# Kernel optimization log

Measured on AMD Instinct MI355X. Metric: run time of the kernel, lower is better.

## Reference

```python
import jax, jax.numpy as jnp
import numpy as np

H = 4  # hidden_size
L = 2  # num_layers


def _lstm_cell(x, h, c, Wih, Whh, bih, bhh):
    # PyTorch gate order: input, forget, cell(g), output
    gates = x @ Wih.T + h @ Whh.T + (bih + bhh)  # [B, 4H]
    i, f, g, o = jnp.split(gates, 4, axis=-1)
    i = jax.nn.sigmoid(i)
    f = jax.nn.sigmoid(f)
    g = jnp.tanh(g)
    o = jax.nn.sigmoid(o)
    c_new = f * c + i * g
    h_new = o * jnp.tanh(c_new)
    return h_new, c_new


def setup_inputs() -> dict:
    key = jax.random.key(0)
    ks = jax.random.split(key, 24)
    B, S, D, T = 32768, 256, 8, 12
    s = 1.0 / np.sqrt(H)  # PyTorch LSTM init scale

    def u(k, shape):
        return jax.random.uniform(k, shape, jnp.float32, -s, s)

    inp = {
        "src": jax.random.normal(ks[0], (B, S, D), jnp.float32),
        "trg": jax.random.normal(ks[1], (B, T, 1), jnp.float32),
        # encoder LSTM (input_dim=8 -> H, then H -> H)
        "enc_Wih0": u(ks[2], (4 * H, D)), "enc_Whh0": u(ks[3], (4 * H, H)),
        "enc_bih0": u(ks[4], (4 * H,)), "enc_bhh0": u(ks[5], (4 * H,)),
        "enc_Wih1": u(ks[6], (4 * H, H)), "enc_Whh1": u(ks[7], (4 * H, H)),
        "enc_bih1": u(ks[8], (4 * H,)), "enc_bhh1": u(ks[9], (4 * H,)),
        # decoder LSTM (input_dim=1 -> H, then H -> H)
        "dec_Wih0": u(ks[10], (4 * H, 1)), "dec_Whh0": u(ks[11], (4 * H, H)),
        "dec_bih0": u(ks[12], (4 * H,)), "dec_bhh0": u(ks[13], (4 * H,)),
        "dec_Wih1": u(ks[14], (4 * H, H)), "dec_Whh1": u(ks[15], (4 * H, H)),
        "dec_bih1": u(ks[16], (4 * H,)), "dec_bhh1": u(ks[17], (4 * H,)),
        # fc: hidden -> 1
        "fc_W": u(ks[18], (1, H)), "fc_b": u(ks[19], (1,)),
    }
    return inp


def reference(src, trg,
              enc_Wih0, enc_Whh0, enc_bih0, enc_bhh0,
              enc_Wih1, enc_Whh1, enc_bih1, enc_bhh1,
              dec_Wih0, dec_Whh0, dec_bih0, dec_bhh0,
              dec_Wih1, dec_Whh1, dec_bih1, dec_bhh1,
              fc_W, fc_b):
    B, T = src.shape[0], trg.shape[1]
    enc_layers = [(enc_Wih0, enc_Whh0, enc_bih0, enc_bhh0),
                  (enc_Wih1, enc_Whh1, enc_bih1, enc_bhh1)]
    dec_layers = [(dec_Wih0, dec_Whh0, dec_bih0, dec_bhh0),
                  (dec_Wih1, dec_Whh1, dec_bih1, dec_bhh1)]

    def multi_step(layers, h, c, x):
        new_h, new_c, inp = [], [], x
        for l, p in enumerate(layers):
            hl, cl = _lstm_cell(inp, h[l], c[l], *p)
            new_h.append(hl); new_c.append(cl); inp = hl
        return jnp.stack(new_h), jnp.stack(new_c), inp

    # ---- encoder: scan over src time steps ----
    h0 = jnp.zeros((L, B, H), src.dtype)
    c0 = jnp.zeros((L, B, H), src.dtype)

    def enc_step(carry, x_t):
        h, c = carry
        h, c, _ = multi_step(enc_layers, h, c, x_t)
        return (h, c), None

    (h, c), _ = jax.lax.scan(enc_step, (h0, c0), jnp.swapaxes(src, 0, 1))

    x0 = trg[:, 0, :]  # [B, 1]

    def dec_step(carry, _):
        h, c, x = carry
        h, c, top = multi_step(dec_layers, h, c, x)
        pred = top @ fc_W.T + fc_b  # [B, 1]
        return (h, c, pred), pred

    _, preds = jax.lax.scan(dec_step, (h, c, x0), None, length=T - 1)  # [T-1, B, 1]
    outputs = jnp.concatenate([x0[None], preds], axis=0)  # [T, B, 1]
    return jnp.swapaxes(outputs, 0, 1)  # [B, T, 1]
```

## Files before the change

### kernel.cpp

```cpp
#include <hip/hip_runtime.h>

namespace {

constexpr int Sn = 256;
constexpr int Tn = 12;
constexpr float L2E = 1.44269504088896340736f;

typedef float v2f __attribute__((ext_vector_type(2)));

__device__ __forceinline__ v2f pkfma(v2f a, v2f b, v2f c) {
  return __builtin_elementwise_fma(a, b, c);
}

__device__ __forceinline__ float rcp_(float x) { return __builtin_amdgcn_rcpf(x); }

#if __has_builtin(__builtin_amdgcn_exp2f)
__device__ __forceinline__ float exp2_(float x) { return __builtin_amdgcn_exp2f(x); }
#else
__device__ __forceinline__ float exp2_(float x) { return __expf(x * 0.69314718055994530942f); }
#endif

template <int CTRL>
__device__ __forceinline__ float qperm(float v) {
  return __int_as_float(
      __builtin_amdgcn_mov_dpp(__float_as_int(v), CTRL, 0xF, 0xF, true));
}
constexpr int DPP_XOR1 = 0xB1;
constexpr int DPP_XOR2 = 0x4E;
constexpr int DPP_XOR3 = 0x1B;
constexpr int DPP_BC0 = 0x00;

__device__ __forceinline__ float unit_update(v2f g01, v2f g23, float& c) {
  float iv = rcp_(1.0f + exp2_(g01.x));
  float fv = rcp_(1.0f + exp2_(g01.y));
  float gv = fmaf(-2.0f, rcp_(exp2_(g23.x) + 1.0f), 1.0f);
  float ov = rcp_(1.0f + exp2_(g23.y));
  c = fmaf(fv, c, iv * gv);
  float th = fmaf(-2.0f, rcp_(exp2_(c * (2.0f * L2E)) + 1.0f), 1.0f);
  return ov * th;
}

__device__ __forceinline__ void quad_gather(float h, float* hg) {
  hg[0] = h;
  hg[1] = qperm<DPP_XOR1>(h);
  hg[2] = qperm<DPP_XOR2>(h);
  hg[3] = qperm<DPP_XOR3>(h);
}

__global__ __launch_bounds__(64, 2) void seq2seq_kernel(
    const float* __restrict__ src, const float* __restrict__ trg,
    const float* __restrict__ eWih0, const float* __restrict__ eWhh0,
    const float* __restrict__ ebih0, const float* __restrict__ ebhh0,
    const float* __restrict__ eWih1, const float* __restrict__ eWhh1,
    const float* __restrict__ ebih1, const float* __restrict__ ebhh1,
    const float* __restrict__ dWih0, const float* __restrict__ dWhh0,
    const float* __restrict__ dbih0, const float* __restrict__ dbhh0,
    const float* __restrict__ dWih1, const float* __restrict__ dWhh1,
    const float* __restrict__ dbih1, const float* __restrict__ dbhh1,
    const float* __restrict__ fcW, const float* __restrict__ fcb,
    float* __restrict__ out) {
  const int gid = blockIdx.x * 64 + threadIdx.x;
  const int e = gid >> 2;
  const int u = gid & 3;

  const int ri = u, rf = 4 + u, rg = 8 + u, ro = 12 + u;

  const v2f s01 = v2f{-L2E, -L2E};
  const v2f s23 = v2f{2.0f * L2E, -L2E};

  v2f w0x01[8], w0x23[8], w0h01[4], w0h23[4];
  v2f w1i01[4], w1i23[4], w1h01[4], w1h23[4];
#pragma unroll
  for (int j = 0; j < 8; ++j) {
    w0x01[j] = v2f{eWih0[ri * 8 + j], eWih0[rf * 8 + j]} * s01;
    w0x23[j] = v2f{eWih0[rg * 8 + j], eWih0[ro * 8 + j]} * s23;
  }
#pragma unroll
  for (int k = 0; k < 4; ++k) {
    const int kc = u ^ k;
    w0h01[k] = v2f{eWhh0[ri * 4 + kc], eWhh0[rf * 4 + kc]} * s01;
    w0h23[k] = v2f{eWhh0[rg * 4 + kc], eWhh0[ro * 4 + kc]} * s23;
    w1i01[k] = v2f{eWih1[ri * 4 + kc], eWih1[rf * 4 + kc]} * s01;
    w1i23[k] = v2f{eWih1[rg * 4 + kc], eWih1[ro * 4 + kc]} * s23;
    w1h01[k] = v2f{eWhh1[ri * 4 + kc], eWhh1[rf * 4 + kc]} * s01;
    w1h23[k] = v2f{eWhh1[rg * 4 + kc], eWhh1[ro * 4 + kc]} * s23;
  }
  const v2f b0_01 = v2f{ebih0[ri] + ebhh0[ri], ebih0[rf] + ebhh0[rf]} * s01;
  const v2f b0_23 = v2f{ebih0[rg] + ebhh0[rg], ebih0[ro] + ebhh0[ro]} * s23;
  const v2f b1_01 = v2f{ebih1[ri] + ebhh1[ri], ebih1[rf] + ebhh1[rf]} * s01;
  const v2f b1_23 = v2f{ebih1[rg] + ebhh1[rg], ebih1[ro] + ebhh1[ro]} * s23;

  const float4* sp = (const float4*)(src + (size_t)e * (Sn * 8));

  float h0g[4] = {0, 0, 0, 0};
  float h1g[4] = {0, 0, 0, 0};
  float c0 = 0.0f, c1 = 0.0f;

  v2f xA01[8], xA23[8], xB01[8], xB23[8];
  float4 raw[16];

  auto convert = [&](int r, v2f& o01, v2f& o23) {
    float4 xa = raw[2 * r], xb = raw[2 * r + 1];
    float x[8] = {xa.x, xa.y, xa.z, xa.w, xb.x, xb.y, xb.z, xb.w};
    v2f a01 = b0_01, a23 = b0_23;
#pragma unroll
    for (int j = 0; j < 8; ++j) {
      v2f xx = v2f{x[j], x[j]};
      a01 = pkfma(xx, w0x01[j], a01);
      a23 = pkfma(xx, w0x23[j], a23);
    }
    o01 = a01;
    o23 = a23;
  };

  auto rstep = [&](v2f a01, v2f a23) {
#pragma unroll
    for (int k = 0; k < 4; ++k) {
      v2f hh = v2f{h0g[k], h0g[k]};
      a01 = pkfma(hh, w0h01[k], a01);
      a23 = pkfma(hh, w0h23[k], a23);
    }
    float h0 = unit_update(a01, a23, c0);
    quad_gather(h0, h0g);

    v2f e01 = b1_01, e23 = b1_23;
#pragma unroll
    for (int k = 0; k < 4; ++k) {
      v2f hh = v2f{h1g[k], h1g[k]};
      e01 = pkfma(hh, w1h01[k], e01);
      e23 = pkfma(hh, w1h23[k], e23);
    }
#pragma unroll
    for (int k = 0; k < 4; ++k) {
      v2f hh = v2f{h0g[k], h0g[k]};
      e01 = pkfma(hh, w1i01[k], e01);
      e23 = pkfma(hh, w1i23[k], e23);
    }
    float h1 = unit_update(e01, e23, c1);
    quad_gather(h1, h1g);
  };

#pragma unroll
  for (int j = 0; j < 16; ++j) raw[j] = sp[j];
#pragma unroll
  for (int r = 0; r < 8; ++r) convert(r, xA01[r], xA23[r]);
#pragma unroll
  for (int j = 0; j < 16; ++j) raw[j] = sp[16 + j];

  for (int i = 0; i < 16; ++i) {
    rstep(xA01[0], xA23[0]);
    rstep(xA01[1], xA23[1]);
    rstep(xA01[2], xA23[2]);
    rstep(xA01[3], xA23[3]);
    rstep(xA01[4], xA23[4]); convert(0, xB01[0], xB23[0]); convert(1, xB01[1], xB23[1]);
    rstep(xA01[5], xA23[5]); convert(2, xB01[2], xB23[2]); convert(3, xB01[3], xB23[3]);
    rstep(xA01[6], xA23[6]); convert(4, xB01[4], xB23[4]); convert(5, xB01[5], xB23[5]);
    rstep(xA01[7], xA23[7]); convert(6, xB01[6], xB23[6]); convert(7, xB01[7], xB23[7]);
    if (i < 15) {
#pragma unroll
      for (int j = 0; j < 16; ++j) raw[j] = sp[32 * (i + 1) + j];
    }
    rstep(xB01[0], xB23[0]);
    rstep(xB01[1], xB23[1]);
    rstep(xB01[2], xB23[2]);
    rstep(xB01[3], xB23[3]);
    if (i < 15) {
      rstep(xB01[4], xB23[4]); convert(0, xA01[0], xA23[0]); convert(1, xA01[1], xA23[1]);
      rstep(xB01[5], xB23[5]); convert(2, xA01[2], xA23[2]); convert(3, xA01[3], xA23[3]);
      rstep(xB01[6], xB23[6]); convert(4, xA01[4], xA23[4]); convert(5, xA01[5], xA23[5]);
      rstep(xB01[7], xB23[7]); convert(6, xA01[6], xA23[6]); convert(7, xA01[7], xA23[7]);
#pragma unroll
      for (int j = 0; j < 16; ++j) raw[j] = sp[32 * (i + 1) + 16 + j];
    } else {
      rstep(xB01[4], xB23[4]);
      rstep(xB01[5], xB23[5]);
      rstep(xB01[6], xB23[6]);
      rstep(xB01[7], xB23[7]);
    }
  }

  v2f dw0i01 = v2f{dWih0[ri], dWih0[rf]} * s01;
  v2f dw0i23 = v2f{dWih0[rg], dWih0[ro]} * s23;
  v2f dw0h01[4], dw0h23[4], dw1i01[4], dw1i23[4], dw1h01[4], dw1h23[4];
#pragma unroll
  for (int k = 0; k < 4; ++k) {
    const int kc = u ^ k;
    dw0h01[k] = v2f{dWhh0[ri * 4 + kc], dWhh0[rf * 4 + kc]} * s01;
    dw0h23[k] = v2f{dWhh0[rg * 4 + kc], dWhh0[ro * 4 + kc]} * s23;
    dw1i01[k] = v2f{dWih1[ri * 4 + kc], dWih1[rf * 4 + kc]} * s01;
    dw1i23[k] = v2f{dWih1[rg * 4 + kc], dWih1[ro * 4 + kc]} * s23;
    dw1h01[k] = v2f{dWhh1[ri * 4 + kc], dWhh1[rf * 4 + kc]} * s01;
    dw1h23[k] = v2f{dWhh1[rg * 4 + kc], dWhh1[ro * 4 + kc]} * s23;
  }
  const v2f db0_01 = v2f{dbih0[ri] + dbhh0[ri], dbih0[rf] + dbhh0[rf]} * s01;
  const v2f db0_23 = v2f{dbih0[rg] + dbhh0[rg], dbih0[ro] + dbhh0[ro]} * s23;
  const v2f db1_01 = v2f{dbih1[ri] + dbhh1[ri], dbih1[rf] + dbhh1[rf]} * s01;
  const v2f db1_23 = v2f{dbih1[rg] + dbhh1[rg], dbih1[ro] + dbhh1[ro]} * s23;
  float fcw[4];
#pragma unroll
  for (int k = 0; k < 4; ++k) fcw[k] = fcW[u ^ k];
  const float fcbv = fcb[0];

  float xv = trg[(size_t)e * Tn];
  if (u == 0) out[(size_t)e * Tn] = xv;

  for (int t = 1; t < Tn; ++t) {
    v2f xx = v2f{xv, xv};
    v2f a01 = pkfma(xx, dw0i01, db0_01);
    v2f a23 = pkfma(xx, dw0i23, db0_23);
#pragma unroll
    for (int k = 0; k < 4; ++k) {
      v2f hh = v2f{h0g[k], h0g[k]};
      a01 = pkfma(hh, dw0h01[k], a01);
      a23 = pkfma(hh, dw0h23[k], a23);
    }
    float h0 = unit_update(a01, a23, c0);
    quad_gather(h0, h0g);

    v2f e01 = db1_01, e23 = db1_23;
#pragma unroll
    for (int k = 0; k < 4; ++k) {
      v2f hh = v2f{h1g[k], h1g[k]};
      e01 = pkfma(hh, dw1h01[k], e01);
      e23 = pkfma(hh, dw1h23[k], e23);
    }
#pragma unroll
    for (int k = 0; k < 4; ++k) {
      v2f hh = v2f{h0g[k], h0g[k]};
      e01 = pkfma(hh, dw1i01[k], e01);
      e23 = pkfma(hh, dw1i23[k], e23);
    }
    float h1 = unit_update(e01, e23, c1);
    quad_gather(h1, h1g);

    float pred = fcbv;
#pragma unroll
    for (int k = 0; k < 4; ++k) pred = fmaf(h1g[k], fcw[k], pred);
    pred = qperm<DPP_BC0>(pred);
    if (u == 0) out[(size_t)e * Tn + t] = pred;
    xv = pred;
  }
}

}

extern "C" void kernel_launch(void* const* d_in, const int* in_sizes, int n_in,
                              void* d_out, int out_size, void* d_ws, size_t ws_size,
                              hipStream_t stream) {
  const float* src = (const float*)d_in[0];
  const float* trg = (const float*)d_in[1];
  const float* eWih0 = (const float*)d_in[2];
  const float* eWhh0 = (const float*)d_in[3];
  const float* ebih0 = (const float*)d_in[4];
  const float* ebhh0 = (const float*)d_in[5];
  const float* eWih1 = (const float*)d_in[6];
  const float* eWhh1 = (const float*)d_in[7];
  const float* ebih1 = (const float*)d_in[8];
  const float* ebhh1 = (const float*)d_in[9];
  const float* dWih0 = (const float*)d_in[10];
  const float* dWhh0 = (const float*)d_in[11];
  const float* dbih0 = (const float*)d_in[12];
  const float* dbhh0 = (const float*)d_in[13];
  const float* dWih1 = (const float*)d_in[14];
  const float* dWhh1 = (const float*)d_in[15];
  const float* dbih1 = (const float*)d_in[16];
  const float* dbhh1 = (const float*)d_in[17];
  const float* fcW = (const float*)d_in[18];
  const float* fcb = (const float*)d_in[19];
  float* out = (float*)d_out;

  const int B = 32768;
  const int lanes = B * 4;
  const int block = 64;
  const int grid = lanes / block;
  seq2seq_kernel<<<grid, block, 0, stream>>>(
      src, trg, eWih0, eWhh0, ebih0, ebhh0, eWih1, eWhh1, ebih1, ebhh1,
      dWih0, dWhh0, dbih0, dbhh0, dWih1, dWhh1, dbih1, dbhh1, fcW, fcb, out);
}
```

Baseline: 517.1 us.

## Merge LSTM gate reciprocals and double-buffer raw inputs with inline projection

New measurement: 443.4 us. 1.17x faster.

```diff
diff --git a/kernel.cpp b/kernel.cpp
--- a/kernel.cpp
+++ b/kernel.cpp
@@ -31,13 +31,15 @@
 constexpr int DPP_BC0 = 0x00;
 
 __device__ __forceinline__ float unit_update(v2f g01, v2f g23, float& c) {
-  float iv = rcp_(1.0f + exp2_(g01.x));
-  float fv = rcp_(1.0f + exp2_(g01.y));
-  float gv = fmaf(-2.0f, rcp_(exp2_(g23.x) + 1.0f), 1.0f);
-  float ov = rcp_(1.0f + exp2_(g23.y));
-  c = fmaf(fv, c, iv * gv);
-  float th = fmaf(-2.0f, rcp_(exp2_(c * (2.0f * L2E)) + 1.0f), 1.0f);
-  return ov * th;
+  float ei = exp2_(g01.x);
+  float ef = exp2_(g01.y);
+  float eg = exp2_(fminf(g23.x, 64.0f));
+  float eo = exp2_(g23.y);
+  float ig = (eg - 1.0f) * rcp_((1.0f + ei) * (eg + 1.0f));
+  float fv = rcp_(1.0f + ef);
+  c = fmaf(fv, c, ig);
+  float ec = exp2_(fminf(c * (2.0f * L2E), 64.0f));
+  return (ec - 1.0f) * rcp_((1.0f + eo) * (ec + 1.0f));
 }
 
 __device__ __forceinline__ void quad_gather(float h, float* hg) {
@@ -47,7 +49,7 @@
   hg[3] = qperm<DPP_XOR3>(h);
 }
 
-__global__ __launch_bounds__(64, 2) void seq2seq_kernel(
+__global__ __launch_bounds__(64) void seq2seq_kernel(
     const float* __restrict__ src, const float* __restrict__ trg,
     const float* __restrict__ eWih0, const float* __restrict__ eWhh0,
     const float* __restrict__ ebih0, const float* __restrict__ ebhh0,
@@ -96,11 +98,7 @@
   float h1g[4] = {0, 0, 0, 0};
   float c0 = 0.0f, c1 = 0.0f;
 
-  v2f xA01[8], xA23[8], xB01[8], xB23[8];
-  float4 raw[16];
-
-  auto convert = [&](int r, v2f& o01, v2f& o23) {
-    float4 xa = raw[2 * r], xb = raw[2 * r + 1];
+  auto enc_step = [&](float4 xa, float4 xb) {
     float x[8] = {xa.x, xa.y, xa.z, xa.w, xb.x, xb.y, xb.z, xb.w};
     v2f a01 = b0_01, a23 = b0_23;
 #pragma unroll
@@ -109,11 +107,6 @@
       a01 = pkfma(xx, w0x01[j], a01);
       a23 = pkfma(xx, w0x23[j], a23);
     }
-    o01 = a01;
-    o23 = a23;
-  };
-
-  auto rstep = [&](v2f a01, v2f a23) {
 #pragma unroll
     for (int k = 0; k < 4; ++k) {
       v2f hh = v2f{h0g[k], h0g[k]};
@@ -140,42 +133,24 @@
     quad_gather(h1, h1g);
   };
 
-#pragma unroll
-  for (int j = 0; j < 16; ++j) raw[j] = sp[j];
-#pragma unroll
-  for (int r = 0; r < 8; ++r) convert(r, xA01[r], xA23[r]);
-#pragma unroll
-  for (int j = 0; j < 16; ++j) raw[j] = sp[16 + j];
+  float4 A[16], B[16];
+#pragma unroll
+  for (int j = 0; j < 16; ++j) A[j] = sp[j];
+#pragma unroll
+  for (int j = 0; j < 16; ++j) B[j] = sp[16 + j];
 
   for (int i = 0; i < 16; ++i) {
-    rstep(xA01[0], xA23[0]);
-    rstep(xA01[1], xA23[1]);
-    rstep(xA01[2], xA23[2]);
-    rstep(xA01[3], xA23[3]);
-    rstep(xA01[4], xA23[4]); convert(0, xB01[0], xB23[0]); convert(1, xB01[1], xB23[1]);
-    rstep(xA01[5], xA23[5]); convert(2, xB01[2], xB23[2]); convert(3, xB01[3], xB23[3]);
-    rstep(xA01[6], xA23[6]); convert(4, xB01[4], xB23[4]); convert(5, xB01[5], xB23[5]);
-    rstep(xA01[7], xA23[7]); convert(6, xB01[6], xB23[6]); convert(7, xB01[7], xB23[7]);
+#pragma unroll
+    for (int s = 0; s < 8; ++s) enc_step(A[2 * s], A[2 * s + 1]);
     if (i < 15) {
 #pragma unroll
-      for (int j = 0; j < 16; ++j) raw[j] = sp[32 * (i + 1) + j];
-    }
-    rstep(xB01[0], xB23[0]);
-    rstep(xB01[1], xB23[1]);
-    rstep(xB01[2], xB23[2]);
-    rstep(xB01[3], xB23[3]);
+      for (int j = 0; j < 16; ++j) A[j] = sp[32 * (i + 1) + j];
+    }
+#pragma unroll
+    for (int s = 0; s < 8; ++s) enc_step(B[2 * s], B[2 * s + 1]);
     if (i < 15) {
-      rstep(xB01[4], xB23[4]); convert(0, xA01[0], xA23[0]); convert(1, xA01[1], xA23[1]);
-      rstep(xB01[5], xB23[5]); convert(2, xA01[2], xA23[2]); convert(3, xA01[3], xA23[3]);
-      rstep(xB01[6], xB23[6]); convert(4, xA01[4], xA23[4]); convert(5, xA01[5], xA23[5]);
-      rstep(xB01[7], xB23[7]); convert(6, xA01[6], xA23[6]); convert(7, xA01[7], xA23[7]);
-#pragma unroll
-      for (int j = 0; j < 16; ++j) raw[j] = sp[32 * (i + 1) + 16 + j];
-    } else {
-      rstep(xB01[4], xB23[4]);
-      rstep(xB01[5], xB23[5]);
-      rstep(xB01[6], xB23[6]);
-      rstep(xB01[7], xB23[7]);
+#pragma unroll
+      for (int j = 0; j < 16; ++j) B[j] = sp[32 * (i + 1) + 16 + j];
     }
   }
 
```
